# Optimization experiments

Measured on AMD Instinct MI355X. Metric: run time of the kernel, lower is better.

## Reference

```python
import jax, jax.numpy as jnp
import numpy as np

EMB = 1024
HID = 4096
B = 2
T = 4096
NUM_BLOCK = 24
EPS = 1e-6


def rmsnorm(x):
    # unparameterized RMS normalization over last dim
    return x * jax.lax.rsqrt(jnp.mean(jnp.square(x), axis=-1, keepdims=True) + EPS)


def setup_inputs() -> dict:
    key = jax.random.key(0)
    k1, k2, k3, k4 = jax.random.split(key, 4)
    x = jax.random.normal(k1, (B, T, EMB), dtype=jnp.float32)
    W1 = 0.02 * jax.random.normal(k2, (HID, EMB), dtype=jnp.float32)
    W2 = 0.02 * jax.random.normal(k3, (HID, EMB), dtype=jnp.float32)
    W3 = (0.02 / np.sqrt(NUM_BLOCK)) * jax.random.normal(k4, (EMB, HID), dtype=jnp.float32)
    return {"x": x, "W1": W1, "W2": W2, "W3": W3}


def bar_quadratic_causal_preact_stable(a, b):
    # y_t = (1/t^2) * sum_{i<=t} sum_{j<=t} exp(a_i + b_j), per feature channel.
    # exp factorizes, so compute stably via log-cumsum-exp along the seq axis.
    seq = a.shape[1]
    log_t = jnp.log(jnp.arange(1, seq + 1, dtype=a.dtype))  # [T]
    la = jax.lax.cumlogsumexp(a, axis=1)  # [B,T,H]
    lb = jax.lax.cumlogsumexp(b, axis=1)  # [B,T,H]
    return jnp.exp(la + lb - 2.0 * log_t[None, :, None])


def reference(x, W1, W2, W3):
    r = rmsnorm(x)
    a = jnp.einsum('bte,he->bth', r, W1)  # fc_1, no bias
    b = jnp.einsum('bte,he->bth', r, W2)  # fc_2, no bias
    r = bar_quadratic_causal_preact_stable(a, b)
    r = rmsnorm(r)
    r = jnp.einsum('bth,eh->bte', r, W3)  # fc_3, no bias
    return x + r
```

## Files before the change

### kernel.cpp

```cpp
#include <hip/hip_runtime.h>
#include <hip/hip_fp8.h>

#define EMB 1024
#define HID 4096
#define NB 2
#define TT 4096
#define MROWS (NB*TT)
#define N1 (2*HID)
#define CHUNK 128
#define NCH 32

typedef short short8 __attribute__((ext_vector_type(8)));
typedef float v4f   __attribute__((ext_vector_type(4)));
typedef int   v4i   __attribute__((ext_vector_type(4)));
typedef int   v8i   __attribute__((ext_vector_type(8)));

__device__ __forceinline__ unsigned short f2bf(float f) {
  unsigned int u = __float_as_uint(f);
  u += 0x7FFFu + ((u >> 16) & 1u);
  return (unsigned short)(u >> 16);
}
__device__ __forceinline__ float bf2f(unsigned short s) {
  return __uint_as_float(((unsigned int)s) << 16);
}
__device__ __forceinline__ unsigned char f2e4m3(float f) {
  __hip_fp8_e4m3 q(f);
  return *(unsigned char*)&q;
}
__device__ __forceinline__ float e4m32f(unsigned char c) {
  __hip_fp8_e4m3 q = *(__hip_fp8_e4m3*)&c;
  return (float)q;
}
__device__ __forceinline__ void g2l16(const void* g, void* l) {
  __builtin_amdgcn_global_load_lds(
      (const __attribute__((address_space(1))) void*)g,
      (__attribute__((address_space(3))) void*)l, 16, 0, 0);
}

__device__ __forceinline__ float block_reduce_sum(float v, float* sbuf) {
  #pragma unroll
  for (int off = 32; off; off >>= 1) v += __shfl_down(v, off, 64);
  int lane = threadIdx.x & 63, w = threadIdx.x >> 6;
  if (lane == 0) sbuf[w] = v;
  __syncthreads();
  return sbuf[0] + sbuf[1] + sbuf[2] + sbuf[3];
}

__global__ __launch_bounds__(256) void conv_all(const float* __restrict__ W1,
                                                const float* __restrict__ W2,
                                                const float* __restrict__ W3,
                                                unsigned short* __restrict__ o12,
                                                unsigned char* __restrict__ o3) {
  size_t i = ((size_t)blockIdx.x*256 + threadIdx.x)*4;
  if (i < 2ull*HID*EMB) {
    const float* s = (i < (size_t)HID*EMB) ? (W1 + i) : (W2 + (i - (size_t)HID*EMB));
    float4 v = *(const float4*)s;
    ushort4 u; u.x=f2bf(v.x); u.y=f2bf(v.y); u.z=f2bf(v.z); u.w=f2bf(v.w);
    *(ushort4*)(o12 + i) = u;
  } else {
    size_t off = i - 2ull*HID*EMB;
    float4 v = *(const float4*)(W3 + off);
    uchar4 u; u.x=f2e4m3(v.x*64.f); u.y=f2e4m3(v.y*64.f);
             u.z=f2e4m3(v.z*64.f); u.w=f2e4m3(v.w*64.f);
    *(uchar4*)(o3 + off) = u;
  }
}

__global__ __launch_bounds__(256) void rmsnorm_x(const float* __restrict__ x,
                                                 unsigned short* __restrict__ r) {
  __shared__ float sbuf[4];
  int row = blockIdx.x;
  float4 v = *(const float4*)(x + (size_t)row*EMB + threadIdx.x*4);
  float ss = v.x*v.x + v.y*v.y + v.z*v.z + v.w*v.w;
  float tot = block_reduce_sum(ss, sbuf);
  float sc = rsqrtf(tot * (1.0f/EMB) + 1e-6f);
  ushort4 o; o.x=f2bf(v.x*sc); o.y=f2bf(v.y*sc); o.z=f2bf(v.z*sc); o.w=f2bf(v.w*sc);
  *(ushort4*)(r + (size_t)row*EMB + threadIdx.x*4) = o;
}

__global__ __launch_bounds__(256, 2)
void gemm_exp(const unsigned short* __restrict__ A,
              const unsigned short* __restrict__ Bt,
              unsigned char* __restrict__ C8,
              float* __restrict__ part,
              int K, int N) {
  __shared__ short lA[128*64];
  __shared__ short lB[128*64];
  const int tid  = threadIdx.x;
  const int lane = tid & 63;
  const int wm   = (tid >> 6) >> 1, wn = (tid >> 6) & 1;
  const int bid  = blockIdx.x;
  const int s0i  = bid >> 3;
  const int rowTile = s0i >> 3;
  const int colTile = ((bid & 7) << 3) | (s0i & 7);
  const int rowBase = rowTile * 128;
  const int colBase = colTile * 128;

  v4f acc[4][4];
  #pragma unroll
  for (int i=0;i<4;++i)
    #pragma unroll
    for (int j=0;j<4;++j) acc[i][j] = (v4f){0.f,0.f,0.f,0.f};

  for (int k0 = 0; k0 < K; k0 += 64) {
    #pragma unroll
    for (int j = 0; j < 4; ++j) {
      int s = j*256 + tid;
      int m = s >> 3;
      int c = (s & 7) ^ (m & 7);
      g2l16(A + (size_t)(rowBase + m)*K + k0 + c*8, &lA[s*8]);
    }
    #pragma unroll
    for (int j = 0; j < 4; ++j) {
      int s = j*256 + tid;
      int m = s >> 3;
      int c = (s & 7) ^ (m & 7);
      g2l16(Bt + (size_t)(colBase + m)*K + k0 + c*8, &lB[s*8]);
    }
    __syncthreads();
    #pragma unroll
    for (int s2 = 0; s2 < 2; ++s2) {
      const int quad = lane >> 4;
      const int cc = s2*4 + quad;
      short8 aF[4], bF[4];
      #pragma unroll
      for (int mt = 0; mt < 4; ++mt) {
        int ml = wm*64 + mt*16 + (lane & 15);
        aF[mt] = *(const short8*)&lA[(ml*8 + (cc ^ (ml & 7)))*8];
      }
      #pragma unroll
      for (int nt = 0; nt < 4; ++nt) {
        int nl = wn*64 + nt*16 + (lane & 15);
        bF[nt] = *(const short8*)&lB[(nl*8 + (cc ^ (nl & 7)))*8];
      }
      #pragma unroll
      for (int mt = 0; mt < 4; ++mt)
        #pragma unroll
        for (int nt = 0; nt < 4; ++nt)
          acc[mt][nt] = __builtin_amdgcn_mfma_f32_16x16x32_bf16(aF[mt], bF[nt], acc[mt][nt], 0, 0, 0);
    }
    __syncthreads();
  }

  const int quad = lane >> 4, c15 = lane & 15;
  float csum[4] = {0.f, 0.f, 0.f, 0.f};
  #pragma unroll
  for (int mt = 0; mt < 4; ++mt) {
    #pragma unroll
    for (int nt = 0; nt < 4; ++nt) {
      int col = colBase + wn*64 + nt*16 + c15;
      #pragma unroll
      for (int r = 0; r < 4; ++r) {
        int row = rowBase + wm*64 + mt*16 + quad*4 + r;
        size_t idx = (size_t)row*N + col;
        float e = __expf(acc[mt][nt][r]);
        C8[idx] = f2e4m3(e);
        csum[nt] += e;
      }
    }
  }
  float* cs = (float*)lA;
  #pragma unroll
  for (int nt = 0; nt < 4; ++nt) {
    float s = csum[nt];
    s += __shfl_xor(s, 16, 64);
    s += __shfl_xor(s, 32, 64);
    if (lane < 16) cs[wm*128 + wn*64 + nt*16 + lane] = s;
  }
  __syncthreads();
  if (tid < 128)
    part[(size_t)(colBase + tid)*64 + rowTile] = cs[tid] + cs[128 + tid];
}

__global__ __launch_bounds__(256, 2)
void gemm_out(const unsigned char* __restrict__ A8,
              const unsigned char* __restrict__ B8,
              const float* __restrict__ x,
              const float* __restrict__ rsq,
              float* __restrict__ out,
              int K, int N) {
  __shared__ unsigned char lA8[128*128];
  __shared__ unsigned char lB8[128*128];
  const int tid  = threadIdx.x;
  const int lane = tid & 63;
  const int wm   = (tid >> 6) >> 1, wn = (tid >> 6) & 1;
  const int rowBase = blockIdx.x * 128;
  const int colBase = blockIdx.y * 128;
  const int q   = lane >> 4;
  const int r15 = lane & 15;

  v4f acc[4][4];
  #pragma unroll
  for (int i=0;i<4;++i)
    #pragma unroll
    for (int j=0;j<4;++j) acc[i][j] = (v4f){0.f,0.f,0.f,0.f};

  for (int k0 = 0; k0 < K; k0 += 128) {
    #pragma unroll
    for (int j = 0; j < 4; ++j) {
      int s = j*256 + tid;
      int m = s >> 3;
      int c = (s & 7) ^ (m & 7);
      g2l16(A8 + (size_t)(rowBase + m)*K + k0 + c*16, &lA8[s*16]);
    }
    #pragma unroll
    for (int j = 0; j < 4; ++j) {
      int s = j*256 + tid;
      int m = s >> 3;
      int c = (s & 7) ^ (m & 7);
      g2l16(B8 + (size_t)(colBase + m)*K + k0 + c*16, &lB8[s*16]);
    }
    __syncthreads();
    v8i aF[4], bF[4];
    #pragma unroll
    for (int mt = 0; mt < 4; ++mt) {
      int ml = wm*64 + mt*16 + r15;
      int s  = ml & 7;
      v4i lo = *(const v4i*)&lA8[ml*128 + (((2*q)   ^ s)<<4)];
      v4i hi = *(const v4i*)&lA8[ml*128 + (((2*q+1) ^ s)<<4)];
      aF[mt] = __builtin_shufflevector(lo, hi, 0,1,2,3,4,5,6,7);
    }
    #pragma unroll
    for (int nt = 0; nt < 4; ++nt) {
      int nl = wn*64 + nt*16 + r15;
      int s  = nl & 7;
      v4i lo = *(const v4i*)&lB8[nl*128 + (((2*q)   ^ s)<<4)];
      v4i hi = *(const v4i*)&lB8[nl*128 + (((2*q+1) ^ s)<<4)];
      bF[nt] = __builtin_shufflevector(lo, hi, 0,1,2,3,4,5,6,7);
    }
    #pragma unroll
    for (int mt = 0; mt < 4; ++mt)
      #pragma unroll
      for (int nt = 0; nt < 4; ++nt)
        acc[mt][nt] = __builtin_amdgcn_mfma_scale_f32_16x16x128_f8f6f4(
            aF[mt], bF[nt], acc[mt][nt],
            0, 0,
            0, 0x7F7F7F7F,
            0, 0x7F7F7F7F);
    __syncthreads();
  }

  const int quad = lane >> 4, c15 = lane & 15;
  #pragma unroll
  for (int mt = 0; mt < 4; ++mt) {
    float scr[4];
    #pragma unroll
    for (int r = 0; r < 4; ++r) {
      int row = rowBase + wm*64 + mt*16 + quad*4 + r;
      scr[r] = rsqrtf(rsq[row]*(1.0f/256.0f) + 1e-6f) * 0.0625f;
    }
    #pragma unroll
    for (int nt = 0; nt < 4; ++nt) {
      int col = colBase + wn*64 + nt*16 + c15;
      #pragma unroll
      for (int r = 0; r < 4; ++r) {
        int row = rowBase + wm*64 + mt*16 + quad*4 + r;
        size_t idx = (size_t)row*N + col;
        out[idx] = x[idx] + scr[r]*acc[mt][nt][r];
      }
    }
  }
}

__global__ __launch_bounds__(256) void scan_prefix(float* __restrict__ part) {
  int idx = blockIdx.x*256 + threadIdx.x;
  int col = idx >> 1, bb = idx & 1;
  float* p = part + (size_t)col*64 + bb*NCH;
  float run = 0.f;
  #pragma unroll
  for (int c = 0; c < NCH; ++c) { float v = p[c]; p[c] = run; run += v; }
}

__global__ __launch_bounds__(256) void scan_emit(const unsigned char* __restrict__ ab,
                                                 const float* __restrict__ part,
                                                 unsigned char* __restrict__ y8) {
  int h0 = (blockIdx.x*256 + threadIdx.x)*4;
  int cy = blockIdx.y, bb = blockIdx.z;
  float sa[4], sb[4];
  #pragma unroll
  for (int j = 0; j < 4; ++j) {
    sa[j] = part[(size_t)(h0+j)*64 + bb*NCH + cy];
    sb[j] = part[(size_t)(HID + h0+j)*64 + bb*NCH + cy];
  }
  const unsigned char* pa = ab + ((size_t)(bb*TT + cy*CHUNK))*N1 + h0;
  const unsigned char* pb = pa + HID;
  unsigned char* py = y8 + ((size_t)(bb*TT + cy*CHUNK))*HID + h0;
  int t0 = cy*CHUNK;
  #pragma unroll 8
  for (int i = 0; i < CHUNK; ++i) {
    uchar4 va = *(const uchar4*)(pa + (size_t)i*N1);
    uchar4 vb = *(const uchar4*)(pb + (size_t)i*N1);
    sa[0] += e4m32f(va.x); sa[1] += e4m32f(va.y);
    sa[2] += e4m32f(va.z); sa[3] += e4m32f(va.w);
    sb[0] += e4m32f(vb.x); sb[1] += e4m32f(vb.y);
    sb[2] += e4m32f(vb.z); sb[3] += e4m32f(vb.w);
    float inv = __builtin_amdgcn_rcpf((float)(t0 + i + 1));
    float i2 = inv*inv*0.25f;
    uchar4 o;
    o.x = f2e4m3(sa[0]*sb[0]*i2); o.y = f2e4m3(sa[1]*sb[1]*i2);
    o.z = f2e4m3(sa[2]*sb[2]*i2); o.w = f2e4m3(sa[3]*sb[3]*i2);
    *(uchar4*)(py + (size_t)i*HID) = o;
  }
}

__global__ __launch_bounds__(256) void rowss(const unsigned char* __restrict__ y8,
                                             float* __restrict__ rsq) {
  __shared__ float sbuf[4];
  int row = blockIdx.x;
  const unsigned char* p = y8 + (size_t)row*HID + threadIdx.x*16;
  uint4 v = *(const uint4*)p;
  float ss = 0.f;
  unsigned int w[4] = {v.x, v.y, v.z, v.w};
  #pragma unroll
  for (int g = 0; g < 4; ++g)
    #pragma unroll
    for (int b = 0; b < 4; ++b) {
      float f = e4m32f((unsigned char)(w[g] >> (8*b)));
      ss += f*f;
    }
  float tot = block_reduce_sum(ss, sbuf);
  if (threadIdx.x == 0) rsq[row] = tot;
}

extern "C" void kernel_launch(void* const* d_in, const int* in_sizes, int n_in,
                              void* d_out, int out_size, void* d_ws, size_t ws_size,
                              hipStream_t stream) {
  const float* x  = (const float*)d_in[0];
  const float* W1 = (const float*)d_in[1];
  const float* W2 = (const float*)d_in[2];
  const float* W3 = (const float*)d_in[3];
  float* out = (float*)d_out;
  char* ws = (char*)d_ws;

  unsigned short* r_bf   = (unsigned short*)(ws);
  unsigned short* w12_bf = (unsigned short*)(ws + 16777216ull);
  unsigned char*  w3_8   = (unsigned char*) (ws + 33554432ull);
  unsigned char*  ab8    = (unsigned char*) (ws + 37748736ull);
  float*          rsq    = (float*)        (ws + 104857600ull);
  unsigned char*  y8     = (unsigned char*) (ws + 171966464ull);
  float*          part   = (float*)d_out;

  conv_all<<<12288, 256, 0, stream>>>(W1, W2, W3, w12_bf, w3_8);
  rmsnorm_x<<<MROWS, 256, 0, stream>>>(x, r_bf);
  gemm_exp<<<4096, 256, 0, stream>>>(r_bf, w12_bf, ab8, part, EMB, N1);
  scan_prefix<<<64, 256, 0, stream>>>(part);
  scan_emit<<<dim3(4,NCH,2), 256, 0, stream>>>(ab8, part, y8);
  rowss<<<MROWS, 256, 0, stream>>>(y8, rsq);
  gemm_out<<<dim3(64,8), 256, 0, stream>>>(y8, w3_8, x, rsq, out, HID, EMB);
}
```

Measured before the change: 335.8 us.

## Store exp activations transposed and scan per-channel over smaller chunks

The first GEMM now writes its exp'd FP8 outputs in a transposed, channel-major layout, packing four consecutive rows into one uchar4 store. The scan kernel then gives each thread one channel and reads 64 contiguous bytes with wide loads. Chunk size is halved to 64, doubling the number of chunks, and per-128-row partial sums are kept at 64-row granularity. This is meant to make scan_emit fully parallel with coalesced loads and to cut the byte-sized scattered stores in the GEMM epilogue. The trade-off is strided transposed stores from the GEMM and per-byte output stores in the scan.

```diff
diff --git a/kernel.cpp b/kernel.cpp
--- a/kernel.cpp
+++ b/kernel.cpp
@@ -7,8 +7,8 @@
 #define TT 4096
 #define MROWS (NB*TT)
 #define N1 (2*HID)
-#define CHUNK 128
-#define NCH 32
+#define CHUNK 64
+#define NCH 64
 
 typedef short short8 __attribute__((ext_vector_type(8)));
 typedef float v4f   __attribute__((ext_vector_type(4)));
@@ -81,7 +81,7 @@
 __global__ __launch_bounds__(256, 2)
 void gemm_exp(const unsigned short* __restrict__ A,
               const unsigned short* __restrict__ Bt,
-              unsigned char* __restrict__ C8,
+              unsigned char* __restrict__ C8T,
               float* __restrict__ part,
               int K, int N) {
   __shared__ short lA[128*64];
@@ -149,14 +149,15 @@
     #pragma unroll
     for (int nt = 0; nt < 4; ++nt) {
       int col = colBase + wn*64 + nt*16 + c15;
-      #pragma unroll
-      for (int r = 0; r < 4; ++r) {
-        int row = rowBase + wm*64 + mt*16 + quad*4 + r;
-        size_t idx = (size_t)row*N + col;
-        float e = __expf(acc[mt][nt][r]);
-        C8[idx] = f2e4m3(e);
-        csum[nt] += e;
-      }
+      int row0 = rowBase + wm*64 + mt*16 + quad*4;
+      float e0 = __expf(acc[mt][nt][0]);
+      float e1 = __expf(acc[mt][nt][1]);
+      float e2 = __expf(acc[mt][nt][2]);
+      float e3 = __expf(acc[mt][nt][3]);
+      csum[nt] += e0 + e1 + e2 + e3;
+      uchar4 o; o.x = f2e4m3(e0); o.y = f2e4m3(e1);
+               o.z = f2e4m3(e2); o.w = f2e4m3(e3);
+      *(uchar4*)(C8T + (size_t)col*MROWS + row0) = o;
     }
   }
   float* cs = (float*)lA;
@@ -168,8 +169,10 @@
     if (lane < 16) cs[wm*128 + wn*64 + nt*16 + lane] = s;
   }
   __syncthreads();
-  if (tid < 128)
-    part[(size_t)(colBase + tid)*64 + rowTile] = cs[tid] + cs[128 + tid];
+  if (tid < 128) {
+    part[(size_t)(colBase + tid)*128 + rowTile*2    ] = cs[tid];
+    part[(size_t)(colBase + tid)*128 + rowTile*2 + 1] = cs[128 + tid];
+  }
 }
 
 __global__ __launch_bounds__(256, 2)
@@ -265,41 +268,38 @@
 __global__ __launch_bounds__(256) void scan_prefix(float* __restrict__ part) {
   int idx = blockIdx.x*256 + threadIdx.x;
   int col = idx >> 1, bb = idx & 1;
-  float* p = part + (size_t)col*64 + bb*NCH;
+  float* p = part + (size_t)col*128 + bb*NCH;
   float run = 0.f;
   #pragma unroll
   for (int c = 0; c < NCH; ++c) { float v = p[c]; p[c] = run; run += v; }
 }
 
-__global__ __launch_bounds__(256) void scan_emit(const unsigned char* __restrict__ ab,
+__global__ __launch_bounds__(256) void scan_emit(const unsigned char* __restrict__ abT,
                                                  const float* __restrict__ part,
                                                  unsigned char* __restrict__ y8) {
-  int h0 = (blockIdx.x*256 + threadIdx.x)*4;
+  int h  = blockIdx.x*256 + threadIdx.x;
   int cy = blockIdx.y, bb = blockIdx.z;
-  float sa[4], sb[4];
+  float sa = part[(size_t)h*128 + bb*NCH + cy];
+  float sb = part[(size_t)(HID + h)*128 + bb*NCH + cy];
+  const unsigned char* pa = abT + (size_t)h*MROWS       + bb*TT + cy*CHUNK;
+  const unsigned char* pb = abT + (size_t)(HID+h)*MROWS + bb*TT + cy*CHUNK;
+  unsigned char* py = y8 + ((size_t)(bb*TT + cy*CHUNK))*HID + h;
+  int t0 = cy*CHUNK;
+
+  uint4 wa[4], wb[4];
   #pragma unroll
   for (int j = 0; j < 4; ++j) {
-    sa[j] = part[(size_t)(h0+j)*64 + bb*NCH + cy];
-    sb[j] = part[(size_t)(HID + h0+j)*64 + bb*NCH + cy];
-  }
-  const unsigned char* pa = ab + ((size_t)(bb*TT + cy*CHUNK))*N1 + h0;
-  const unsigned char* pb = pa + HID;
-  unsigned char* py = y8 + ((size_t)(bb*TT + cy*CHUNK))*HID + h0;
-  int t0 = cy*CHUNK;
-  #pragma unroll 8
+    wa[j] = *(const uint4*)(pa + j*16);
+    wb[j] = *(const uint4*)(pb + j*16);
+  }
+  #pragma unroll
   for (int i = 0; i < CHUNK; ++i) {
-    uchar4 va = *(const uchar4*)(pa + (size_t)i*N1);
-    uchar4 vb = *(const uchar4*)(pb + (size_t)i*N1);
-    sa[0] += e4m32f(va.x); sa[1] += e4m32f(va.y);
-    sa[2] += e4m32f(va.z); sa[3] += e4m32f(va.w);
-    sb[0] += e4m32f(vb.x); sb[1] += e4m32f(vb.y);
-    sb[2] += e4m32f(vb.z); sb[3] += e4m32f(vb.w);
+    const int k = i >> 4, w = (i >> 2) & 3, sh = (i & 3)*8;
+    unsigned int ua = (&wa[k].x)[w], ub = (&wb[k].x)[w];
+    sa += e4m32f((unsigned char)(ua >> sh));
+    sb += e4m32f((unsigned char)(ub >> sh));
     float inv = __builtin_amdgcn_rcpf((float)(t0 + i + 1));
-    float i2 = inv*inv*0.25f;
-    uchar4 o;
-    o.x = f2e4m3(sa[0]*sb[0]*i2); o.y = f2e4m3(sa[1]*sb[1]*i2);
-    o.z = f2e4m3(sa[2]*sb[2]*i2); o.w = f2e4m3(sa[3]*sb[3]*i2);
-    *(uchar4*)(py + (size_t)i*HID) = o;
+    py[(size_t)i*HID] = f2e4m3(sa*sb*inv*inv*0.25f);
   }
 }
 
@@ -335,16 +335,16 @@
   unsigned short* r_bf   = (unsigned short*)(ws);
   unsigned short* w12_bf = (unsigned short*)(ws + 16777216ull);
   unsigned char*  w3_8   = (unsigned char*) (ws + 33554432ull);
-  unsigned char*  ab8    = (unsigned char*) (ws + 37748736ull);
+  unsigned char*  ab8T   = (unsigned char*) (ws + 37748736ull);
   float*          rsq    = (float*)        (ws + 104857600ull);
   unsigned char*  y8     = (unsigned char*) (ws + 171966464ull);
   float*          part   = (float*)d_out;
 
   conv_all<<<12288, 256, 0, stream>>>(W1, W2, W3, w12_bf, w3_8);
   rmsnorm_x<<<MROWS, 256, 0, stream>>>(x, r_bf);
-  gemm_exp<<<4096, 256, 0, stream>>>(r_bf, w12_bf, ab8, part, EMB, N1);
+  gemm_exp<<<4096, 256, 0, stream>>>(r_bf, w12_bf, ab8T, part, EMB, N1);
   scan_prefix<<<64, 256, 0, stream>>>(part);
-  scan_emit<<<dim3(4,NCH,2), 256, 0, stream>>>(ab8, part, y8);
+  scan_emit<<<dim3(16,NCH,2), 256, 0, stream>>>(ab8T, part, y8);
   rowss<<<MROWS, 256, 0, stream>>>(y8, rsq);
   gemm_out<<<dim3(64,8), 256, 0, stream>>>(y8, w3_8, x, rsq, out, HID, EMB);
 }
```

Result: slower. 362.3 us (+7.9%).
